# Performance work log

Measured on AMD Instinct MI355X. Metric: run time of the kernel, lower is better.

The kernel has to match this reference:

```python
import jax, jax.numpy as jnp
import numpy as np

N = 20          # n_qubits
L = 4           # n_layers
B = 4           # batch of states
DIM = 1 << N    # 2^N = 1048576

_H = jnp.asarray((1.0 / np.sqrt(2.0)) * np.array([[1.0, 1.0], [1.0, -1.0]]), dtype=jnp.complex64)


def _apply_1q(psi, U, q):
    # psi: [B, 2^N]; apply 2x2 unitary U on big-endian qubit q
    left = 1 << q
    right = 1 << (N - q - 1)
    out = jnp.einsum('uv,blvr->blur', U, psi.reshape(-1, left, 2, right))
    return out.reshape(-1, DIM)


def _apply_cnot(psi, control, target):
    ctrl_mask = np.uint32(1 << (N - 1 - control))
    targ_mask = np.uint32(1 << (N - 1 - target))
    idx = jnp.arange(DIM, dtype=jnp.uint32)
    perm = jnp.where((idx & ctrl_mask) != 0, idx ^ targ_mask, idx)
    return psi[:, perm]


def _rot_x(theta):
    c = jnp.cos(theta / 2.0).astype(jnp.complex64)
    s = (-1j * jnp.sin(theta / 2.0)).astype(jnp.complex64)
    return jnp.stack([jnp.stack([c, s]), jnp.stack([s, c])])


def _rot_z(theta):
    e = jnp.exp(-0.5j * theta.astype(jnp.complex64))
    z = jnp.zeros((), jnp.complex64)
    return jnp.stack([jnp.stack([e, z]), jnp.stack([z, jnp.conj(e)])])


def _circuit(psi, thetas_x, thetas_z):
    for q in range(N):
        psi = _apply_1q(psi, _H, q)
    for l in range(L):
        for q in range(N):
            psi = _apply_1q(psi, _rot_z(thetas_z[l, q]), q)
        for q in range(N):
            psi = _apply_1q(psi, _rot_x(thetas_x[l, q]), q)
        for q in range(N - 1):  # linear entanglement
            psi = _apply_cnot(psi, q, q + 1)
    return psi


def setup_inputs() -> dict:
    key = jax.random.key(0)
    k1, k2, k3, k4 = jax.random.split(key, 4)
    return {
        'psi0_real': jax.random.normal(k1, (B, DIM), dtype=jnp.float32),
        'psi0_imag': jax.random.normal(k2, (B, DIM), dtype=jnp.float32),
        'thetas_x': jax.random.normal(k3, (L, N), dtype=jnp.float32),
        'thetas_z': jax.random.normal(k4, (L, N), dtype=jnp.float32),
    }


def reference(psi0_real, psi0_imag, thetas_x, thetas_z):
    psi = (psi0_real + 1j * psi0_imag).astype(jnp.complex64)
    return _circuit(psi, thetas_x, thetas_z)
```

## Files before the change

### kernel.cpp

```cpp
#include <hip/hip_runtime.h>
#include <math.h>


#define NQ 20

struct U2 { float r00,i00,r01,i01,r10,i10,r11,i11; };

__device__ __forceinline__ U2 make_u(const float* __restrict__ thx,
                                     const float* __restrict__ thz,
                                     int layer, int q, int withH) {
  float tx = 0.5f * thx[layer*NQ + q];
  float tz = 0.5f * thz[layer*NQ + q];
  float sx, cxv; __sincosf(tx, &sx, &cxv);
  float sz, cz;  __sincosf(tz, &sz, &cz);
  U2 u;
  u.r00 =  cxv*cz;  u.i00 = -cxv*sz;
  u.r01 =  sx*sz;   u.i01 = -sx*cz;
  u.r10 = -sx*sz;   u.i10 = -sx*cz;
  u.r11 =  cxv*cz;  u.i11 =  cxv*sz;
  if (withH) {
    const float r = 0.70710678118654752f;
    float a, b;
    a=u.r00; b=u.r01; u.r00=(a+b)*r; u.r01=(a-b)*r;
    a=u.i00; b=u.i01; u.i00=(a+b)*r; u.i01=(a-b)*r;
    a=u.r10; b=u.r11; u.r10=(a+b)*r; u.r11=(a-b)*r;
    a=u.i10; b=u.i11; u.i10=(a+b)*r; u.i11=(a-b)*r;
  }
  return u;
}

template <int ST>
__device__ __forceinline__ void bfly8(float* re, float* im, const U2 u) {
#pragma unroll
  for (int s = 0; s < 8; ++s) {
    if ((s & ST) == 0) {
      const int s1 = s + ST;
      float ar = re[s], ai = im[s], br = re[s1], bi = im[s1];
      re[s]  = u.r00*ar - u.i00*ai + u.r01*br - u.i01*bi;
      im[s]  = u.r00*ai + u.i00*ar + u.r01*bi + u.i01*br;
      re[s1] = u.r10*ar - u.i10*ai + u.r11*br - u.i11*bi;
      im[s1] = u.r10*ai + u.i10*ar + u.r11*bi + u.i11*br;
    }
  }
}

template <int ST>
__device__ __forceinline__ void bfly8_rx(float* re, float* im, float c, float s) {
#pragma unroll
  for (int k = 0; k < 8; ++k) {
    if ((k & ST) == 0) {
      const int k1 = k + ST;
      float ar = re[k], ai = im[k], br = re[k1], bi = im[k1];
      re[k]  = c*ar + s*bi;
      im[k]  = c*ai - s*br;
      re[k1] = c*br + s*ai;
      im[k1] = c*bi - s*ar;
    }
  }
}

template <int RXONLY, int ST>
__device__ __forceinline__ void gate8(float* re, float* im,
                                      const float* __restrict__ thx,
                                      const float* __restrict__ thz,
                                      int layer, int q, int withH) {
  if (RXONLY) {
    float sx, cx; __sincosf(0.5f * thx[layer*NQ + q], &sx, &cx);
    bfly8_rx<ST>(re, im, cx, sx);
  } else {
    bfly8<ST>(re, im, make_u(thx, thz, layer, q, withH));
  }
}

__device__ __forceinline__ int K(int j) { return j ^ (((j >> 6) & 0xF) << 2); }

__device__ __forceinline__ unsigned pkbf(float a, float b) {
  unsigned r;
  asm("v_cvt_pk_bf16_f32 %0, %1, %2" : "=v"(r) : "v"(a), "v"(b));
  return r;
}
__device__ __forceinline__ float blo(unsigned p) { return __uint_as_float(p << 16); }
__device__ __forceinline__ float bhi(unsigned p) { return __uint_as_float(p & 0xFFFF0000u); }

__device__ __forceinline__ void unpack_g(uint4 v, float* re, float* im) {
  re[0]=blo(v.x); re[1]=bhi(v.x); re[2]=blo(v.y); re[3]=bhi(v.y);
  im[0]=blo(v.z); im[1]=bhi(v.z); im[2]=blo(v.w); im[3]=bhi(v.w);
}

template <int FIN, int RXONLY>
__global__ __launch_bounds__(512, 8) void pass_a(
    uint4* __restrict__ ws, float* __restrict__ outre,
    const float* __restrict__ thx, const float* __restrict__ thz,
    int layer, int withH) {
  __shared__ __align__(16) float sre[4096];
  __shared__ __align__(16) float sim[4096];
  float4* sre4 = (float4*)sre;
  float4* sim4 = (float4*)sim;
  const int t = threadIdx.x;
  const int b = blockIdx.x >> 8;
  const int m = blockIdx.x & 255;
  const size_t base = (((size_t)b) << NQ) | ((size_t)m << 12);
  float re[8], im[8];
  const int j0 = t << 3;

#pragma unroll
  for (int g2 = 0; g2 < 2; ++g2)
    unpack_g(ws[(base + j0 + (g2 << 2)) >> 2], re + 4*g2, im + 4*g2);
  gate8<RXONLY,1>(re, im, thx, thz, layer, 19, withH);
  gate8<RXONLY,2>(re, im, thx, thz, layer, 18, withH);
  gate8<RXONLY,4>(re, im, thx, thz, layer, 17, withH);

  const int F0 = (t << 1) ^ ((t >> 3) & 0xF);
#pragma unroll
  for (int g2 = 0; g2 < 2; ++g2) {
    int F = F0 ^ g2;
    sre4[F] = make_float4(re[4*g2+0], re[4*g2+1], re[4*g2+2], re[4*g2+3]);
    sim4[F] = make_float4(im[4*g2+0], im[4*g2+1], im[4*g2+2], im[4*g2+3]);
  }
  __syncthreads();

  const int b2 = (t & 7) | ((t >> 3) << 6);
  const int base2 = b2 ^ (((t >> 3) & 0xF) << 2);
#pragma unroll
  for (int e = 0; e < 8; ++e) { int k = base2 ^ (e << 3); re[e]=sre[k]; im[e]=sim[k]; }
  gate8<RXONLY,1>(re, im, thx, thz, layer, 16, withH);
  gate8<RXONLY,2>(re, im, thx, thz, layer, 15, withH);
  gate8<RXONLY,4>(re, im, thx, thz, layer, 14, withH);
#pragma unroll
  for (int e = 0; e < 8; ++e) { int k = base2 ^ (e << 3); sre[k]=re[e]; sim[k]=im[e]; }
  __syncthreads();

  const int b3 = (t & 63) | ((t >> 6) << 9);
  const int base3 = b3 ^ (((t >> 6) & 1) << 5);
#pragma unroll
  for (int e = 0; e < 8; ++e) { int k = base3 ^ ((e << 6) | (e << 2)); re[e]=sre[k]; im[e]=sim[k]; }
  gate8<RXONLY,1>(re, im, thx, thz, layer, 13, withH);
  gate8<RXONLY,2>(re, im, thx, thz, layer, 12, withH);
  gate8<RXONLY,4>(re, im, thx, thz, layer, 11, withH);
#pragma unroll
  for (int e = 0; e < 8; ++e) { int k = base3 ^ ((e << 6) | (e << 2)); sre[k]=re[e]; sim[k]=im[e]; }
  __syncthreads();

  const int base4 = t ^ (((t >> 6) & 7) << 2);
#pragma unroll
  for (int e = 0; e < 8; ++e) { int k = base4 ^ ((e << 9) | ((e & 1) << 5)); re[e]=sre[k]; im[e]=sim[k]; }
  gate8<RXONLY,1>(re, im, thx, thz, layer, 10, withH);
  gate8<RXONLY,2>(re, im, thx, thz, layer,  9, withH);
  gate8<RXONLY,4>(re, im, thx, thz, layer,  8, withH);
#pragma unroll
  for (int e = 0; e < 8; ++e) { int k = base4 ^ ((e << 9) | ((e & 1) << 5)); sre[k]=re[e]; sim[k]=im[e]; }
  __syncthreads();

  const int c11 = (m & 1) << 11;
#pragma unroll
  for (int g2 = 0; g2 < 2; ++g2) {
    int y0 = j0 | (g2 << 2);
    int x0 = y0 ^ ((y0 >> 1) & 0x7FF) ^ c11;
    int FG = K(x0 & ~3) >> 2;
    float4 vr = sre4[FG], vi = sim4[FG];
    if (x0 & 2) {
      vr = make_float4(vr.z, vr.w, vr.x, vr.y);
      vi = make_float4(vi.z, vi.w, vi.x, vi.y);
    }
    if (FIN) {
      *(float4*)(outre + base + y0) = make_float4(vr.x, vr.y, vr.w, vr.z);
    } else {
      uint4 v;
      v.x = pkbf(vr.x, vr.y); v.y = pkbf(vr.w, vr.z);
      v.z = pkbf(vi.x, vi.y); v.w = pkbf(vi.w, vi.z);
      ws[(base + y0) >> 2] = v;
    }
  }
}

template <int INIT, int DIAG>
__global__ __launch_bounds__(512, 8) void pass_b(
    const float* __restrict__ in_re, const float* __restrict__ in_im,
    uint4* __restrict__ ws,
    const float* __restrict__ thx, const float* __restrict__ thz,
    int layer, int withH) {
  __shared__ __align__(16) float sre[4096];
  __shared__ __align__(16) float sim[4096];
  float4* sre4 = (float4*)sre;
  float4* sim4 = (float4*)sim;
  const int t = threadIdx.x;
  const int b = blockIdx.x >> 8;
  const int m = blockIdx.x & 255;
  const size_t base = ((size_t)b) << NQ;
  float re[8], im[8];
  const int j0 = t << 3;

  float pb = 0.f, z19 = 0.f, z18 = 0.f, z17 = 0.f;
  if (DIAG) {
    const float* Z = thz + layer*NQ;
    float s0 = 0.f;
#pragma unroll
    for (int q = 0; q < NQ; ++q) s0 += Z[q];
    pb = -0.5f * s0;
#pragma unroll
    for (int k = 0; k < 8; ++k)
      pb += (m & (1 << k)) ? Z[15 - k] : 0.f;
    pb += (t & 1) ? Z[16] : 0.f;
#pragma unroll
    for (int k = 1; k <= 8; ++k)
      pb += (t & (1 << k)) ? Z[8 - k] : 0.f;
    z19 = Z[19]; z18 = Z[18]; z17 = Z[17];
  }

#pragma unroll
  for (int g2 = 0; g2 < 2; ++g2) {
    int y = j0 | (g2 << 2);
    int g0 = ((y >> 4) << 12) | (m << 4) | (y & 15);
    if (INIT) {
      float4 vr = *(const float4*)(in_re + base + g0);
      float4 vi = *(const float4*)(in_im + base + g0);
      re[4*g2+0]=vr.x; re[4*g2+1]=vr.y; re[4*g2+2]=vr.z; re[4*g2+3]=vr.w;
      im[4*g2+0]=vi.x; im[4*g2+1]=vi.y; im[4*g2+2]=vi.z; im[4*g2+3]=vi.w;
    } else {
      unpack_g(ws[(base + g0) >> 2], re + 4*g2, im + 4*g2);
    }
  }
  if (DIAG) {
#pragma unroll
    for (int s = 0; s < 8; ++s) {
      float ang = pb + ((s & 1) ? z19 : 0.f) + ((s & 2) ? z18 : 0.f)
                     + ((s & 4) ? z17 : 0.f);
      float sn, cs; __sincosf(ang, &sn, &cs);
      float r0 = re[s], i0 = im[s];
      re[s] = cs*r0 - sn*i0;
      im[s] = cs*i0 + sn*r0;
    }
  }

  const int F0 = (t << 1) ^ ((t >> 3) & 0xF);
#pragma unroll
  for (int g2 = 0; g2 < 2; ++g2) {
    int F = F0 ^ g2;
    sre4[F] = make_float4(re[4*g2+0], re[4*g2+1], re[4*g2+2], re[4*g2+3]);
    sim4[F] = make_float4(im[4*g2+0], im[4*g2+1], im[4*g2+2], im[4*g2+3]);
  }
  __syncthreads();

  const int b2 = (t & 15) | ((t >> 4) << 7);
  const int baseB2 = b2 ^ (((t >> 4) & 7) << 3);
#pragma unroll
  for (int e = 0; e < 8; ++e) { int k = baseB2 ^ ((e << 4) | ((e >> 2) << 2)); re[e]=sre[k]; im[e]=sim[k]; }
  gate8<DIAG,1>(re, im, thx, thz, layer, 7, withH);
  gate8<DIAG,2>(re, im, thx, thz, layer, 6, withH);
  gate8<DIAG,4>(re, im, thx, thz, layer, 5, withH);
#pragma unroll
  for (int e = 0; e < 8; ++e) { int k = baseB2 ^ ((e << 4) | ((e >> 2) << 2)); sre[k]=re[e]; sim[k]=im[e]; }
  __syncthreads();

  const int b3 = (t & 127) | ((t >> 7) << 10);
  const int baseB3 = b3 ^ (((t >> 6) & 1) << 2);
#pragma unroll
  for (int e = 0; e < 8; ++e) { int k = baseB3 ^ ((e << 7) | (e << 3)); re[e]=sre[k]; im[e]=sim[k]; }
  gate8<DIAG,1>(re, im, thx, thz, layer, 4, withH);
  gate8<DIAG,2>(re, im, thx, thz, layer, 3, withH);
  gate8<DIAG,4>(re, im, thx, thz, layer, 2, withH);
#pragma unroll
  for (int e = 0; e < 8; ++e) { int k = baseB3 ^ ((e << 7) | (e << 3)); sre[k]=re[e]; sim[k]=im[e]; }
  __syncthreads();

  const int base4 = t ^ (((t >> 6) & 7) << 2);
#pragma unroll
  for (int e = 0; e < 8; ++e) { int k = base4 ^ ((e << 9) | ((e & 1) << 5)); re[e]=sre[k]; im[e]=sim[k]; }
  gate8<DIAG,2>(re, im, thx, thz, layer, 1, withH);
  gate8<DIAG,4>(re, im, thx, thz, layer, 0, withH);
#pragma unroll
  for (int e = 0; e < 8; ++e) { int k = base4 ^ ((e << 9) | ((e & 1) << 5)); sre[k]=re[e]; sim[k]=im[e]; }
  __syncthreads();

#pragma unroll
  for (int g2 = 0; g2 < 2; ++g2) {
    int y0 = j0 | (g2 << 2);
    int x0 = y0 ^ ((y0 >> 1) & 0x7F0);
    int FG = K(x0) >> 2;
    float4 vr = sre4[FG], vi = sim4[FG];
    int g0 = ((y0 >> 4) << 12) | (m << 4) | (y0 & 15);
    uint4 v;
    v.x = pkbf(vr.x, vr.y); v.y = pkbf(vr.z, vr.w);
    v.z = pkbf(vi.x, vi.y); v.w = pkbf(vi.z, vi.w);
    ws[(base + g0) >> 2] = v;
  }
}

extern "C" void kernel_launch(void* const* d_in, const int* in_sizes, int n_in,
                              void* d_out, int out_size, void* d_ws, size_t ws_size,
                              hipStream_t stream) {
  const float* p_re = (const float*)d_in[0];
  const float* p_im = (const float*)d_in[1];
  const float* thx  = (const float*)d_in[2];
  const float* thz  = (const float*)d_in[3];
  float* outre = (float*)d_out;
  uint4* ws = (uint4*)d_ws;

  dim3 grid(1024), blk(512);
  pass_b<1,0><<<grid, blk, 0, stream>>>(p_re, p_im, ws, thx, thz, 0, 1);
  pass_a<0,0><<<grid, blk, 0, stream>>>(ws, outre, thx, thz, 0, 1);
  for (int l = 1; l < 3; ++l) {
    pass_b<0,1><<<grid, blk, 0, stream>>>(nullptr, nullptr, ws, thx, thz, l, 0);
    pass_a<0,1><<<grid, blk, 0, stream>>>(ws, outre, thx, thz, l, 0);
  }
  pass_b<0,1><<<grid, blk, 0, stream>>>(nullptr, nullptr, ws, thx, thz, 3, 0);
  pass_a<1,1><<<grid, blk, 0, stream>>>(ws, outre, thx, thz, 3, 0);
}
```

Before: 206.1 us.

## Ping-pong workspace buffers with transposed layout and nontemporal loads/stores

Adds nontemporal load/store helpers for all global state traffic. When the workspace is large enough, it switches to two ping-pong buffers. pass_a then writes its output in the layout pass_b wants to read, so pass_b reads contiguous rows instead of strided gathers. This aims to make pass_b's input reads coalesced and to cut cache pollution, at the cost of doubling workspace use and a scattered write pattern in pass_a.

```diff
diff --git a/kernel.cpp b/kernel.cpp
--- a/kernel.cpp
+++ b/kernel.cpp
@@ -5,6 +5,26 @@
 #define NQ 20
 
 struct U2 { float r00,i00,r01,i01,r10,i10,r11,i11; };
+
+typedef unsigned int u32x4 __attribute__((ext_vector_type(4)));
+typedef float        f32x4 __attribute__((ext_vector_type(4)));
+
+__device__ __forceinline__ uint4 ld_nt4(const uint4* p) {
+  u32x4 v = __builtin_nontemporal_load((const u32x4*)p);
+  uint4 r; r.x = v[0]; r.y = v[1]; r.z = v[2]; r.w = v[3]; return r;
+}
+__device__ __forceinline__ void st_nt4(uint4* p, uint4 v) {
+  u32x4 t; t[0] = v.x; t[1] = v.y; t[2] = v.z; t[3] = v.w;
+  __builtin_nontemporal_store(t, (u32x4*)p);
+}
+__device__ __forceinline__ float4 ldf_nt4(const float* p) {
+  f32x4 v = __builtin_nontemporal_load((const f32x4*)p);
+  return make_float4(v[0], v[1], v[2], v[3]);
+}
+__device__ __forceinline__ void stf_nt4(float* p, float4 v) {
+  f32x4 t; t[0] = v.x; t[1] = v.y; t[2] = v.z; t[3] = v.w;
+  __builtin_nontemporal_store(t, (f32x4*)p);
+}
 
 __device__ __forceinline__ U2 make_u(const float* __restrict__ thx,
                                      const float* __restrict__ thz,
@@ -87,9 +107,10 @@
   im[0]=blo(v.z); im[1]=bhi(v.z); im[2]=blo(v.w); im[3]=bhi(v.w);
 }
 
-template <int FIN, int RXONLY>
+template <int FIN, int RXONLY, int PP>
 __global__ __launch_bounds__(512, 8) void pass_a(
-    uint4* __restrict__ ws, float* __restrict__ outre,
+    const uint4* __restrict__ src, uint4* __restrict__ dst,
+    float* __restrict__ outre,
     const float* __restrict__ thx, const float* __restrict__ thz,
     int layer, int withH) {
   __shared__ __align__(16) float sre[4096];
@@ -105,7 +126,7 @@
 
 #pragma unroll
   for (int g2 = 0; g2 < 2; ++g2)
-    unpack_g(ws[(base + j0 + (g2 << 2)) >> 2], re + 4*g2, im + 4*g2);
+    unpack_g(ld_nt4(src + ((base + j0 + (g2 << 2)) >> 2)), re + 4*g2, im + 4*g2);
   gate8<RXONLY,1>(re, im, thx, thz, layer, 19, withH);
   gate8<RXONLY,2>(re, im, thx, thz, layer, 18, withH);
   gate8<RXONLY,4>(re, im, thx, thz, layer, 17, withH);
@@ -163,20 +184,27 @@
       vi = make_float4(vi.z, vi.w, vi.x, vi.y);
     }
     if (FIN) {
-      *(float4*)(outre + base + y0) = make_float4(vr.x, vr.y, vr.w, vr.z);
+      stf_nt4(outre + base + y0, make_float4(vr.x, vr.y, vr.w, vr.z));
     } else {
       uint4 v;
       v.x = pkbf(vr.x, vr.y); v.y = pkbf(vr.w, vr.z);
       v.z = pkbf(vi.x, vi.y); v.w = pkbf(vi.w, vi.z);
-      ws[(base + y0) >> 2] = v;
-    }
-  }
-}
-
-template <int INIT, int DIAG>
+      size_t n;
+      if (PP) {
+        n = (((size_t)b) << NQ) | ((size_t)m << 4)
+          | (size_t)((y0 & 15) | ((y0 >> 4) << 12));
+      } else {
+        n = base + y0;
+      }
+      st_nt4(dst + (n >> 2), v);
+    }
+  }
+}
+
+template <int INIT, int DIAG, int PP>
 __global__ __launch_bounds__(512, 8) void pass_b(
     const float* __restrict__ in_re, const float* __restrict__ in_im,
-    uint4* __restrict__ ws,
+    const uint4* __restrict__ src, uint4* __restrict__ dst,
     const float* __restrict__ thx, const float* __restrict__ thz,
     int layer, int withH) {
   __shared__ __align__(16) float sre[4096];
@@ -209,15 +237,20 @@
 
 #pragma unroll
   for (int g2 = 0; g2 < 2; ++g2) {
-    int y = j0 | (g2 << 2);
-    int g0 = ((y >> 4) << 12) | (m << 4) | (y & 15);
     if (INIT) {
-      float4 vr = *(const float4*)(in_re + base + g0);
-      float4 vi = *(const float4*)(in_im + base + g0);
+      int y = j0 | (g2 << 2);
+      int g0 = ((y >> 4) << 12) | (m << 4) | (y & 15);
+      float4 vr = ldf_nt4(in_re + base + g0);
+      float4 vi = ldf_nt4(in_im + base + g0);
       re[4*g2+0]=vr.x; re[4*g2+1]=vr.y; re[4*g2+2]=vr.z; re[4*g2+3]=vr.w;
       im[4*g2+0]=vi.x; im[4*g2+1]=vi.y; im[4*g2+2]=vi.z; im[4*g2+3]=vi.w;
+    } else if (PP) {
+      size_t nB = base | ((size_t)m << 12) | (size_t)(j0 | (g2 << 2));
+      unpack_g(ld_nt4(src + (nB >> 2)), re + 4*g2, im + 4*g2);
     } else {
-      unpack_g(ws[(base + g0) >> 2], re + 4*g2, im + 4*g2);
+      int y = j0 | (g2 << 2);
+      int g0 = ((y >> 4) << 12) | (m << 4) | (y & 15);
+      unpack_g(ld_nt4(src + ((base + g0) >> 2)), re + 4*g2, im + 4*g2);
     }
   }
   if (DIAG) {
@@ -282,7 +315,7 @@
     uint4 v;
     v.x = pkbf(vr.x, vr.y); v.y = pkbf(vr.z, vr.w);
     v.z = pkbf(vi.x, vi.y); v.w = pkbf(vi.z, vi.w);
-    ws[(base + g0) >> 2] = v;
+    st_nt4(dst + ((base + g0) >> 2), v);
   }
 }
 
@@ -294,15 +327,29 @@
   const float* thx  = (const float*)d_in[2];
   const float* thz  = (const float*)d_in[3];
   float* outre = (float*)d_out;
-  uint4* ws = (uint4*)d_ws;
+  const size_t HALF = (size_t)16 << 20;
+  uint4* ws0 = (uint4*)d_ws;
+  uint4* ws1 = (uint4*)((char*)d_ws + HALF);
 
   dim3 grid(1024), blk(512);
-  pass_b<1,0><<<grid, blk, 0, stream>>>(p_re, p_im, ws, thx, thz, 0, 1);
-  pass_a<0,0><<<grid, blk, 0, stream>>>(ws, outre, thx, thz, 0, 1);
-  for (int l = 1; l < 3; ++l) {
-    pass_b<0,1><<<grid, blk, 0, stream>>>(nullptr, nullptr, ws, thx, thz, l, 0);
-    pass_a<0,1><<<grid, blk, 0, stream>>>(ws, outre, thx, thz, l, 0);
-  }
-  pass_b<0,1><<<grid, blk, 0, stream>>>(nullptr, nullptr, ws, thx, thz, 3, 0);
-  pass_a<1,1><<<grid, blk, 0, stream>>>(ws, outre, thx, thz, 3, 0);
-}
+
+  if (ws_size >= 2 * HALF) {
+    pass_b<1,0,1><<<grid, blk, 0, stream>>>(p_re, p_im, nullptr, ws0, thx, thz, 0, 1);
+    pass_a<0,0,1><<<grid, blk, 0, stream>>>(ws0, ws1, outre, thx, thz, 0, 1);
+    for (int l = 1; l < 3; ++l) {
+      pass_b<0,1,1><<<grid, blk, 0, stream>>>(nullptr, nullptr, ws1, ws0, thx, thz, l, 0);
+      pass_a<0,1,1><<<grid, blk, 0, stream>>>(ws0, ws1, outre, thx, thz, l, 0);
+    }
+    pass_b<0,1,1><<<grid, blk, 0, stream>>>(nullptr, nullptr, ws1, ws0, thx, thz, 3, 0);
+    pass_a<1,1,1><<<grid, blk, 0, stream>>>(ws0, nullptr, outre, thx, thz, 3, 0);
+  } else {
+    pass_b<1,0,0><<<grid, blk, 0, stream>>>(p_re, p_im, nullptr, ws0, thx, thz, 0, 1);
+    pass_a<0,0,0><<<grid, blk, 0, stream>>>(ws0, ws0, outre, thx, thz, 0, 1);
+    for (int l = 1; l < 3; ++l) {
+      pass_b<0,1,0><<<grid, blk, 0, stream>>>(nullptr, nullptr, ws0, ws0, thx, thz, l, 0);
+      pass_a<0,1,0><<<grid, blk, 0, stream>>>(ws0, ws0, outre, thx, thz, l, 0);
+    }
+    pass_b<0,1,0><<<grid, blk, 0, stream>>>(nullptr, nullptr, ws0, ws0, thx, thz, 3, 0);
+    pass_a<1,1,0><<<grid, blk, 0, stream>>>(ws0, nullptr, outre, thx, thz, 3, 0);
+  }
+}
```

After: 199.1 us. 1.03x faster.
